# Kernel optimization log

Measured on AMD Instinct MI355X. Metric: run time of the kernel, lower is better.

The kernel has to match this reference:

```python
import jax, jax.numpy as jnp
import numpy as np
import math

B, S, D = 2, 2048, 2048
HQ, HKV = 16, 4            # query heads, kv heads
HD = D // HQ               # head dim = 128
REPS = HQ // HKV           # queries per kv head = 4
KVD = HKV * HD             # 512


def setup_inputs() -> dict:
    key = jax.random.key(0)
    ks = jax.random.split(key, 7)
    s = 0.02
    return {
        "hidden_states": jax.random.normal(ks[0], (B, S, D), dtype=jnp.float32),
        "Wq": jax.random.normal(ks[1], (D, D), dtype=jnp.float32) * s,
        "bq": jnp.zeros((D,), dtype=jnp.float32),
        "Wk": jax.random.normal(ks[2], (D, KVD), dtype=jnp.float32) * s,
        "bk": jnp.zeros((KVD,), dtype=jnp.float32),
        "Wv": jax.random.normal(ks[3], (D, KVD), dtype=jnp.float32) * s,
        "bv": jnp.zeros((KVD,), dtype=jnp.float32),
    }


def reference(hidden_states, Wq, bq, Wk, bk, Wv, bv):
    b, s, d = hidden_states.shape
    # Projections
    q = hidden_states @ Wq + bq                      # [B,S,D]
    k = hidden_states @ Wk + bk                      # [B,S,KVD]
    v = hidden_states @ Wv + bv                      # [B,S,KVD]
    # Split heads. torch repeat_kv_heads uses .repeat (tile), so expanded
    # head h maps to kv head (h mod HKV). Reshape q heads as (REPS, HKV)
    # so axis g indexes the kv head, matching that tiling exactly.
    q = q.reshape(b, s, HQ, HD).transpose(0, 2, 1, 3)          # [B,HQ,S,hd]
    q = q.reshape(b, REPS, HKV, s, HD)                          # [B,R,G,S,hd]
    k = k.reshape(b, s, HKV, HD).transpose(0, 2, 1, 3)          # [B,G,S,hd]
    v = v.reshape(b, s, HKV, HD).transpose(0, 2, 1, 3)          # [B,G,S,hd]
    scale = 1.0 / math.sqrt(HD)
    scores = jnp.einsum('brgsd,bgtd->brgst', q, k) * scale      # [B,R,G,S,S]
    probs = jax.nn.softmax(scores, axis=-1)
    ctx = jnp.einsum('brgst,bgtd->brgsd', probs, v)             # [B,R,G,S,hd]
    ctx = ctx.reshape(b, HQ, s, HD).transpose(0, 2, 1, 3)       # [B,S,HQ,hd]
    return ctx.reshape(b, s, HQ * HD)                            # [B,S,D]
```

## Files before the change

kernel.cpp:

```cpp
#include <hip/hip_runtime.h>
#include <hip/hip_bf16.h>

#define QSCALE   0.08838834764831845f
#define QKSCALE  0.1275174468755322f

typedef __attribute__((ext_vector_type(8))) short bh8;
typedef __attribute__((ext_vector_type(4))) float fx4;
typedef __attribute__((ext_vector_type(4))) short sh4;

typedef const __attribute__((address_space(1))) unsigned GAu;
typedef __attribute__((address_space(3))) unsigned LAu;

__device__ __forceinline__ short f2bf(float f) {
    unsigned u = __float_as_uint(f);
    unsigned r = u + 0x7fffu + ((u >> 16) & 1u);
    return (short)(r >> 16);
}

__device__ __forceinline__ unsigned pk_bf16(float x, float y) {
    union { __hip_bfloat162 h; unsigned u; } cv;
    cv.h = __float22bfloat162_rn(float2{x, y});
    return cv.u;
}

__global__ __launch_bounds__(256) void cvt_x(const float* __restrict__ x,
                                             short* __restrict__ o) {
    int i = blockIdx.x * 256 + threadIdx.x;
    float4 v = ((const float4*)x)[i];
    sh4 s;
    s.x = f2bf(v.x); s.y = f2bf(v.y); s.z = f2bf(v.z); s.w = f2bf(v.w);
    ((sh4*)o)[i] = s;
}

__global__ __launch_bounds__(256) void transpose_w(const float* __restrict__ w,
                                                   short* __restrict__ wt,
                                                   int K, int N) {
    __shared__ float tile[32][33];
    int nb = blockIdx.x, kb = blockIdx.y;
    int tx = threadIdx.x & 31, ty = threadIdx.x >> 5;
#pragma unroll
    for (int j = 0; j < 4; ++j) {
        int k = kb * 32 + ty + j * 8;
        tile[ty + j * 8][tx] = w[(size_t)k * N + nb * 32 + tx];
    }
    __syncthreads();
#pragma unroll
    for (int j = 0; j < 4; ++j) {
        int n = nb * 32 + ty + j * 8;
        wt[(size_t)n * K + kb * 32 + tx] = f2bf(tile[tx][ty + j * 8]);
    }
}

__global__ __launch_bounds__(256) void proj_gemm(
    const short* __restrict__ X,
    const short* __restrict__ WqT,
    const short* __restrict__ WkT,
    const short* __restrict__ WvT,
    const float* __restrict__ bq, const float* __restrict__ bk,
    const float* __restrict__ bv,
    short* __restrict__ Qb, short* __restrict__ Kpk, short* __restrict__ Vpk) {
    __shared__ short As[128 * 32];
    __shared__ short Bs[128 * 32];

    const int tid = threadIdx.x;
    const int bm = blockIdx.x;
    const int ntg = blockIdx.y;

    const short* Wm; const float* bias; int col0, kind;
    if (ntg < 16)      { Wm = WqT; bias = bq; col0 = ntg * 128;        kind = 0; }
    else if (ntg < 20) { Wm = WkT; bias = bk; col0 = (ntg - 16) * 128; kind = 1; }
    else               { Wm = WvT; bias = bv; col0 = (ntg - 20) * 128; kind = 2; }

    const int w = tid >> 6, lane = tid & 63, quad = lane >> 4, l16 = lane & 15;

    fx4 acc[2][8];
#pragma unroll
    for (int i = 0; i < 2; ++i)
#pragma unroll
        for (int j = 0; j < 8; ++j) acc[i][j] = fx4{0.f, 0.f, 0.f, 0.f};

    const int srow = w * 16 + (lane >> 2);
    const int scol = (((lane & 3) ^ ((lane >> 2) & 3)) * 8);
    const short* Ag = X + (size_t)(bm * 128 + srow) * 2048 + scol;
    const short* Bg = Wm + (size_t)(col0 + srow) * 2048 + scol;
    short* AsW = As + w * 512;
    short* BsW = Bs + w * 512;

    const int fchunk = (quad ^ (l16 & 3)) * 8;
    const short* afp0 = As + (w * 32 + l16) * 32 + fchunk;
    const short* afp1 = As + (w * 32 + 16 + l16) * 32 + fchunk;

    for (int kt = 0; kt < 64; ++kt) {
        const int k0 = kt * 32;
        __syncthreads();
#pragma unroll
        for (int j = 0; j < 2; ++j) {
            __builtin_amdgcn_global_load_lds((GAu*)(Ag + (size_t)(j * 64) * 2048 + k0),
                                             (LAu*)(AsW + j * 2048), 16, 0, 0);
            __builtin_amdgcn_global_load_lds((GAu*)(Bg + (size_t)(j * 64) * 2048 + k0),
                                             (LAu*)(BsW + j * 2048), 16, 0, 0);
        }
        __syncthreads();
        bh8 af0 = *(const bh8*)afp0;
        bh8 af1 = *(const bh8*)afp1;
#pragma unroll
        for (int nt = 0; nt < 8; ++nt) {
            bh8 bf = *(const bh8*)(Bs + (nt * 16 + l16) * 32 + fchunk);
            acc[0][nt] = __builtin_amdgcn_mfma_f32_16x16x32_bf16(af0, bf, acc[0][nt], 0, 0, 0);
            acc[1][nt] = __builtin_amdgcn_mfma_f32_16x16x32_bf16(af1, bf, acc[1][nt], 0, 0, 0);
        }
    }

#pragma unroll
    for (int mt = 0; mt < 2; ++mt) {
        int srow2 = bm * 128 + w * 32 + mt * 16 + quad * 4;
#pragma unroll
        for (int nt = 0; nt < 8; ++nt) {
            int c = col0 + nt * 16 + l16;
            float bval = bias[c];
#pragma unroll
            for (int r = 0; r < 4; ++r) {
                int sg = srow2 + r;
                int b = sg >> 11, s = sg & 2047;
                float v = acc[mt][nt][r] + bval;
                int hd = c & 127;
                if (kind == 0) {
                    v *= QKSCALE;
                    int h = c >> 7;
                    Qb[(((size_t)(b * 16 + h) * 2048 + s) << 7) + hd] = f2bf(v);
                } else if (kind == 1) {
                    int g = c >> 7;
                    int ktt = s >> 6, tl = s & 63;
                    int fnt = tl >> 4, fl16 = tl & 15;
                    int ks = hd >> 5, qd = (hd >> 3) & 3, j = hd & 7;
                    size_t frag = (((size_t)(b * 4 + g) * 32 + ktt) * 16 + fnt * 4 + ks);
                    Kpk[frag * 512 + (qd * 16 + fl16) * 8 + j] = f2bf(v);
                } else {
                    int g = c >> 7;
                    int ktt = s >> 6, tl = s & 63;
                    int ts = tl >> 5, qd = (tl >> 3) & 3, j = tl & 7;
                    int fnt = hd >> 4, fl16 = hd & 15;
                    size_t frag = (((size_t)(b * 4 + g) * 32 + ktt) * 16 + fnt * 2 + ts);
                    Vpk[frag * 512 + (qd * 16 + fl16) * 8 + j] = f2bf(v);
                }
            }
        }
    }
}

__global__ __launch_bounds__(256, 4) void attn(
    const short* __restrict__ Qb,
    const short* __restrict__ Kpk,
    const short* __restrict__ Vpk,
    float* __restrict__ out) {
    __shared__ short Ks[2][8 * 512];
    __shared__ short Vs[2][8 * 512];
    __shared__ __align__(16) unsigned Ps[4][16][20];

    const int bid = blockIdx.x;
    const int gb = bid & 7;
    const int rep = (bid >> 3) & 3;
    const int qt = bid >> 5;
    const int b = gb >> 2, g = gb & 3;
    const int h = rep * 4 + g;
    const int tid = threadIdx.x, w = tid >> 6, lane = tid & 63;
    const int quad = lane >> 4, l16 = lane & 15;

    bh8 qf[4];
    {
        int s = qt * 64 + w * 16 + l16;
        const short* qp = Qb + (((size_t)(b * 16 + h) * 2048 + s) << 7);
#pragma unroll
        for (int ks = 0; ks < 4; ++ks)
            qf[ks] = *(const bh8*)(qp + ks * 32 + quad * 8);
    }

    const short* kbase = Kpk + ((size_t)gb * 32) * 8192;
    const short* vbase = Vpk + ((size_t)gb * 32) * 8192;

    fx4 ctx[8];
#pragma unroll
    for (int j = 0; j < 8; ++j) ctx[j] = fx4{0.f, 0.f, 0.f, 0.f};
    float l_part[4] = {0.f, 0.f, 0.f, 0.f};

#pragma unroll
    for (int i = 0; i < 2; ++i) {
        int f = w * 2 + i;
        __builtin_amdgcn_global_load_lds((GAu*)(kbase + f * 512 + lane * 8),
                                         (LAu*)(&Ks[0][f * 512]), 16, 0, 0);
        __builtin_amdgcn_global_load_lds((GAu*)(vbase + (size_t)f * 1024 + lane * 8),
                                         (LAu*)(&Vs[0][f * 512]), 16, 0, 0);
    }
    __syncthreads();

    for (int kt = 0; kt < 64; ++kt) {
        const int cur = kt & 1;

        if (kt < 63) {
            const int kn = kt + 1;
            const short* kp = kbase + (size_t)kn * 4096;
            const short* vp = vbase + (size_t)(kn >> 1) * 8192 + (kn & 1) * 512;
#pragma unroll
            for (int i = 0; i < 2; ++i) {
                int f = w * 2 + i;
                __builtin_amdgcn_global_load_lds((GAu*)(kp + f * 512 + lane * 8),
                                                 (LAu*)(&Ks[cur ^ 1][f * 512]), 16, 0, 0);
                __builtin_amdgcn_global_load_lds((GAu*)(vp + (size_t)f * 1024 + lane * 8),
                                                 (LAu*)(&Vs[cur ^ 1][f * 512]), 16, 0, 0);
            }
        }

        fx4 sc[2];
        sc[0] = fx4{0.f, 0.f, 0.f, 0.f};
        sc[1] = fx4{0.f, 0.f, 0.f, 0.f};
#pragma unroll
        for (int nti = 0; nti < 2; ++nti) {
#pragma unroll
            for (int ks = 0; ks < 4; ++ks) {
                bh8 kf = *(const bh8*)(&Ks[cur][(nti * 4 + ks) * 512] + lane * 8);
                sc[nti] = __builtin_amdgcn_mfma_f32_16x16x32_bf16(qf[ks], kf, sc[nti], 0, 0, 0);
            }
        }

#pragma unroll
        for (int r = 0; r < 4; ++r) {
            float p0 = __builtin_amdgcn_exp2f(sc[0][r]);
            float p1 = __builtin_amdgcn_exp2f(sc[1][r]);
            l_part[r] += p0 + p1;
            Ps[w][quad * 4 + r][l16] = pk_bf16(p0, p1);
        }

        bh8 pa;
        {
            const unsigned* prow = &Ps[w][l16][(quad & 1) * 8];
            uint4 lo = *(const uint4*)(prow);
            uint4 hi = *(const uint4*)(prow + 4);
            unsigned dw[8] = {lo.x, lo.y, lo.z, lo.w, hi.x, hi.y, hi.z, hi.w};
            unsigned sel = (quad & 2) ? 0x07060302u : 0x05040100u;
            unsigned a[4];
#pragma unroll
            for (int j = 0; j < 4; ++j)
                a[j] = __builtin_amdgcn_perm(dw[2 * j + 1], dw[2 * j], sel);
            pa = *(const bh8*)a;
        }

#pragma unroll
        for (int nt = 0; nt < 8; ++nt) {
            bh8 vf = *(const bh8*)(&Vs[cur][nt * 512] + lane * 8);
            ctx[nt] = __builtin_amdgcn_mfma_f32_16x16x32_bf16(pa, vf, ctx[nt], 0, 0, 0);
        }

        __syncthreads();
    }

    {
        int srow = qt * 64 + w * 16 + quad * 4;
#pragma unroll
        for (int r = 0; r < 4; ++r) {
            float lsum = l_part[r];
            lsum += __shfl_xor(lsum, 1);
            lsum += __shfl_xor(lsum, 2);
            lsum += __shfl_xor(lsum, 4);
            lsum += __shfl_xor(lsum, 8);
            float inv = 1.f / lsum;
            size_t rowoff = ((size_t)b * 2048 + (srow + r)) * 2048 + h * 128;
#pragma unroll
            for (int nt = 0; nt < 8; ++nt)
                out[rowoff + nt * 16 + l16] = ctx[nt][r] * inv;
        }
    }
}

extern "C" void kernel_launch(void* const* d_in, const int* in_sizes, int n_in,
                              void* d_out, int out_size, void* d_ws, size_t ws_size,
                              hipStream_t stream) {
    const float* hs = (const float*)d_in[0];
    const float* Wq = (const float*)d_in[1];
    const float* bq = (const float*)d_in[2];
    const float* Wk = (const float*)d_in[3];
    const float* bk = (const float*)d_in[4];
    const float* Wv = (const float*)d_in[5];
    const float* bv = (const float*)d_in[6];
    float* out = (float*)d_out;

    char* ws = (char*)d_ws;
    short* Xbf = (short*)(ws);
    short* WqT = (short*)(ws + 16777216);
    short* WkT = (short*)(ws + 25165824);
    short* WvT = (short*)(ws + 27262976);
    short* Qb  = (short*)(ws + 29360128);
    short* Kpk = (short*)(ws + 46137344);
    short* Vpk = (short*)(ws + 50331648);

    cvt_x<<<8192, 256, 0, stream>>>(hs, Xbf);
    transpose_w<<<dim3(64, 64), 256, 0, stream>>>(Wq, WqT, 2048, 2048);
    transpose_w<<<dim3(16, 64), 256, 0, stream>>>(Wk, WkT, 2048, 512);
    transpose_w<<<dim3(16, 64), 256, 0, stream>>>(Wv, WvT, 2048, 512);
    proj_gemm<<<dim3(32, 24), 256, 0, stream>>>(Xbf, WqT, WkT, WvT, bq, bk, bv,
                                                Qb, Kpk, Vpk);
    attn<<<1024, 256, 0, stream>>>(Qb, Kpk, Vpk, out);
}
```

Measured before the change: 285.6 us.

## Double-buffer LDS tiles in projection GEMM to overlap loads with MFMA

The projection GEMM now keeps two LDS buffers for the A and B tiles. It prefetches tile k+1 with global_load_lds while the MFMAs run on tile k, which cuts the two barriers per k-step down to one. The goal is to hide global memory latency behind matrix math. In exchange, LDS use per block doubles, which may lower occupancy, and the barrier at the end of each iteration still waits for the outstanding prefetch.

```diff
diff --git a/kernel.cpp b/kernel.cpp
--- a/kernel.cpp
+++ b/kernel.cpp
@@ -59,8 +59,8 @@
     const float* __restrict__ bq, const float* __restrict__ bk,
     const float* __restrict__ bv,
     short* __restrict__ Qb, short* __restrict__ Kpk, short* __restrict__ Vpk) {
-    __shared__ short As[128 * 32];
-    __shared__ short Bs[128 * 32];
+    __shared__ short As[2][128 * 32];
+    __shared__ short Bs[2][128 * 32];
 
     const int tid = threadIdx.x;
     const int bm = blockIdx.x;
@@ -83,32 +83,45 @@
     const int scol = (((lane & 3) ^ ((lane >> 2) & 3)) * 8);
     const short* Ag = X + (size_t)(bm * 128 + srow) * 2048 + scol;
     const short* Bg = Wm + (size_t)(col0 + srow) * 2048 + scol;
-    short* AsW = As + w * 512;
-    short* BsW = Bs + w * 512;
+    const int stoff = w * 512;
 
     const int fchunk = (quad ^ (l16 & 3)) * 8;
-    const short* afp0 = As + (w * 32 + l16) * 32 + fchunk;
-    const short* afp1 = As + (w * 32 + 16 + l16) * 32 + fchunk;
+    const int aoff0 = (w * 32 + l16) * 32 + fchunk;
+    const int aoff1 = (w * 32 + 16 + l16) * 32 + fchunk;
+
+#pragma unroll
+    for (int j = 0; j < 2; ++j) {
+        __builtin_amdgcn_global_load_lds((GAu*)(Ag + (size_t)(j * 64) * 2048),
+                                         (LAu*)(&As[0][stoff + j * 2048]), 16, 0, 0);
+        __builtin_amdgcn_global_load_lds((GAu*)(Bg + (size_t)(j * 64) * 2048),
+                                         (LAu*)(&Bs[0][stoff + j * 2048]), 16, 0, 0);
+    }
+    __syncthreads();
 
     for (int kt = 0; kt < 64; ++kt) {
-        const int k0 = kt * 32;
-        __syncthreads();
-#pragma unroll
-        for (int j = 0; j < 2; ++j) {
-            __builtin_amdgcn_global_load_lds((GAu*)(Ag + (size_t)(j * 64) * 2048 + k0),
-                                             (LAu*)(AsW + j * 2048), 16, 0, 0);
-            __builtin_amdgcn_global_load_lds((GAu*)(Bg + (size_t)(j * 64) * 2048 + k0),
-                                             (LAu*)(BsW + j * 2048), 16, 0, 0);
-        }
-        __syncthreads();
-        bh8 af0 = *(const bh8*)afp0;
-        bh8 af1 = *(const bh8*)afp1;
+        const int cur = kt & 1;
+
+        if (kt < 63) {
+            const int k0 = (kt + 1) * 32;
+#pragma unroll
+            for (int j = 0; j < 2; ++j) {
+                __builtin_amdgcn_global_load_lds((GAu*)(Ag + (size_t)(j * 64) * 2048 + k0),
+                                                 (LAu*)(&As[cur ^ 1][stoff + j * 2048]), 16, 0, 0);
+                __builtin_amdgcn_global_load_lds((GAu*)(Bg + (size_t)(j * 64) * 2048 + k0),
+                                                 (LAu*)(&Bs[cur ^ 1][stoff + j * 2048]), 16, 0, 0);
+            }
+        }
+
+        bh8 af0 = *(const bh8*)(&As[cur][aoff0]);
+        bh8 af1 = *(const bh8*)(&As[cur][aoff1]);
 #pragma unroll
         for (int nt = 0; nt < 8; ++nt) {
-            bh8 bf = *(const bh8*)(Bs + (nt * 16 + l16) * 32 + fchunk);
+            bh8 bf = *(const bh8*)(&Bs[cur][(nt * 16 + l16) * 32 + fchunk]);
             acc[0][nt] = __builtin_amdgcn_mfma_f32_16x16x32_bf16(af0, bf, acc[0][nt], 0, 0, 0);
             acc[1][nt] = __builtin_amdgcn_mfma_f32_16x16x32_bf16(af1, bf, acc[1][nt], 0, 0, 0);
         }
+
+        __syncthreads();
     }
 
 #pragma unroll
```

New measurement: 302.1 us. 5.8% more time.

## Double-buffer LDS tiles in projection GEMM to overlap loads with MFMA

Applied to the files above, without the earlier changes.

The projection GEMM now uses two LDS buffers each for the A and B tiles. The main loop issues the async global-to-LDS copy for the next k-tile before running the MFMAs on the current one, and needs one barrier per tile instead of two. The goal is to hide global load latency behind matrix math in this stage. In exchange the kernel doubles its LDS footprint (32 KB per block), which can reduce the number of blocks resident per CU.

```diff
diff --git a/kernel.cpp b/kernel.cpp
--- a/kernel.cpp
+++ b/kernel.cpp
@@ -59,8 +59,10 @@
     const float* __restrict__ bq, const float* __restrict__ bk,
     const float* __restrict__ bv,
     short* __restrict__ Qb, short* __restrict__ Kpk, short* __restrict__ Vpk) {
-    __shared__ short As[128 * 32];
-    __shared__ short Bs[128 * 32];
+    __shared__ short As0[128 * 32];
+    __shared__ short As1[128 * 32];
+    __shared__ short Bs0[128 * 32];
+    __shared__ short Bs1[128 * 32];
 
     const int tid = threadIdx.x;
     const int bm = blockIdx.x;
@@ -83,33 +85,57 @@
     const int scol = (((lane & 3) ^ ((lane >> 2) & 3)) * 8);
     const short* Ag = X + (size_t)(bm * 128 + srow) * 2048 + scol;
     const short* Bg = Wm + (size_t)(col0 + srow) * 2048 + scol;
-    short* AsW = As + w * 512;
-    short* BsW = Bs + w * 512;
+    const int stoff = w * 512;
 
     const int fchunk = (quad ^ (l16 & 3)) * 8;
-    const short* afp0 = As + (w * 32 + l16) * 32 + fchunk;
-    const short* afp1 = As + (w * 32 + 16 + l16) * 32 + fchunk;
-
-    for (int kt = 0; kt < 64; ++kt) {
-        const int k0 = kt * 32;
+    const int aoff0 = (w * 32 + l16) * 32 + fchunk;
+    const int aoff1 = aoff0 + 512;
+    const int boff  = l16 * 32 + fchunk;
+
+    const short* pA00 = As0 + aoff0;  const short* pA01 = As0 + aoff1;
+    const short* pA10 = As1 + aoff0;  const short* pA11 = As1 + aoff1;
+    const short* pB0  = Bs0 + boff;   const short* pB1  = Bs1 + boff;
+
+#define PG_STAGE(AsD, BsD, ktile)                                               \
+    do {                                                                        \
+        const int k0_ = (ktile) * 32;                                           \
+        _Pragma("unroll")                                                       \
+        for (int j = 0; j < 2; ++j) {                                           \
+            __builtin_amdgcn_global_load_lds(                                   \
+                (GAu*)(Ag + (size_t)(j * 64) * 2048 + k0_),                     \
+                (LAu*)(AsD + stoff + j * 2048), 16, 0, 0);                      \
+            __builtin_amdgcn_global_load_lds(                                   \
+                (GAu*)(Bg + (size_t)(j * 64) * 2048 + k0_),                     \
+                (LAu*)(BsD + stoff + j * 2048), 16, 0, 0);                      \
+        }                                                                       \
+    } while (0)
+
+#define PG_COMPUTE(pA0_, pA1_, pB_)                                             \
+    do {                                                                        \
+        bh8 af0 = *(const bh8*)(pA0_);                                          \
+        bh8 af1 = *(const bh8*)(pA1_);                                          \
+        _Pragma("unroll")                                                       \
+        for (int nt = 0; nt < 8; ++nt) {                                        \
+            bh8 bf = *(const bh8*)((pB_) + nt * 512);                           \
+            acc[0][nt] = __builtin_amdgcn_mfma_f32_16x16x32_bf16(af0, bf, acc[0][nt], 0, 0, 0); \
+            acc[1][nt] = __builtin_amdgcn_mfma_f32_16x16x32_bf16(af1, bf, acc[1][nt], 0, 0, 0); \
+        }                                                                       \
+    } while (0)
+
+    PG_STAGE(As0, Bs0, 0);
+    __syncthreads();
+
+    for (int kt = 0; kt < 64; kt += 2) {
+        PG_STAGE(As1, Bs1, kt + 1);
+        PG_COMPUTE(pA00, pA01, pB0);
         __syncthreads();
-#pragma unroll
-        for (int j = 0; j < 2; ++j) {
-            __builtin_amdgcn_global_load_lds((GAu*)(Ag + (size_t)(j * 64) * 2048 + k0),
-                                             (LAu*)(AsW + j * 2048), 16, 0, 0);
-            __builtin_amdgcn_global_load_lds((GAu*)(Bg + (size_t)(j * 64) * 2048 + k0),
-                                             (LAu*)(BsW + j * 2048), 16, 0, 0);
-        }
+
+        if (kt < 62) PG_STAGE(As0, Bs0, kt + 2);
+        PG_COMPUTE(pA10, pA11, pB1);
         __syncthreads();
-        bh8 af0 = *(const bh8*)afp0;
-        bh8 af1 = *(const bh8*)afp1;
-#pragma unroll
-        for (int nt = 0; nt < 8; ++nt) {
-            bh8 bf = *(const bh8*)(Bs + (nt * 16 + l16) * 32 + fchunk);
-            acc[0][nt] = __builtin_amdgcn_mfma_f32_16x16x32_bf16(af0, bf, acc[0][nt], 0, 0, 0);
-            acc[1][nt] = __builtin_amdgcn_mfma_f32_16x16x32_bf16(af1, bf, acc[1][nt], 0, 0, 0);
-        }
-    }
+    }
+#undef PG_STAGE
+#undef PG_COMPUTE
 
 #pragma unroll
     for (int mt = 0; mt < 2; ++mt) {
```

Measured after the change: 275.9 us. -3.4%, faster.
